# Kernel tuning notes

Hardware: AMD Instinct MI355X
Metric: run time of the kernel (lower is better)

Reference implementation:

```python
import jax, jax.numpy as jnp
import numpy as np

B, N, D_IN, D_OUT, H = 64, 512, 256, 256, 4
HD = D_OUT // H


def setup_inputs() -> dict:
    key = jax.random.key(0)
    ks = jax.random.split(key, 10)
    x = jax.random.normal(ks[0], (B, N, D_IN), dtype=jnp.float32)
    adj = jax.random.randint(ks[1], (N, N), 0, 2, dtype=jnp.int32)
    adj = adj.at[jnp.arange(N), jnp.arange(N)].set(1)  # self-loops: no empty rows
    s_in = 1.0 / np.sqrt(D_IN)
    s_out = 1.0 / np.sqrt(D_OUT)
    wq = jax.random.uniform(ks[2], (D_OUT, D_IN), jnp.float32, -s_in, s_in)
    bq = jax.random.uniform(ks[3], (D_OUT,), jnp.float32, -s_in, s_in)
    wk = jax.random.uniform(ks[4], (D_OUT, D_IN), jnp.float32, -s_in, s_in)
    bk = jax.random.uniform(ks[5], (D_OUT,), jnp.float32, -s_in, s_in)
    wv = jax.random.uniform(ks[6], (D_OUT, D_IN), jnp.float32, -s_in, s_in)
    bv = jax.random.uniform(ks[7], (D_OUT,), jnp.float32, -s_in, s_in)
    wo = jax.random.uniform(ks[8], (D_OUT, D_OUT), jnp.float32, -s_out, s_out)
    bo = jax.random.uniform(ks[9], (D_OUT,), jnp.float32, -s_out, s_out)
    return {"x": x, "adj": adj, "wq": wq, "bq": bq, "wk": wk, "bk": bk,
            "wv": wv, "bv": bv, "wo": wo, "bo": bo}


def reference(x, adj, wq, bq, wk, bk, wv, bv, wo, bo):
    b, n, _ = x.shape
    # [B,N,D_out] -> [B,H,N,HD]
    q = (x @ wq.T + bq).reshape(b, n, H, HD).transpose(0, 2, 1, 3)
    k = (x @ wk.T + bk).reshape(b, n, H, HD).transpose(0, 2, 1, 3)
    v = (x @ wv.T + bv).reshape(b, n, H, HD).transpose(0, 2, 1, 3)
    scores = jnp.einsum('bhnd,bhmd->bhnm', q, k) / jnp.sqrt(jnp.float32(HD))
    scores = jnp.where(adj[None, None] == 0, -jnp.inf, scores)
    attn = jnp.nan_to_num(jax.nn.softmax(scores, axis=-1), nan=0.0)
    out = jnp.einsum('bhnm,bhmd->bhnd', attn, v)
    out = out.transpose(0, 2, 1, 3).reshape(b, n, D_OUT)
    return out @ wo.T + bo
```

## Files before the change

kernel.cpp:

```cpp
#include <hip/hip_runtime.h>
#include <stdint.h>

typedef float f32x4 __attribute__((ext_vector_type(4)));
typedef short s16x8 __attribute__((ext_vector_type(8)));
typedef unsigned short u16x4 __attribute__((ext_vector_type(4)));

#define BB 64
#define NN 512
#define DIN 256
#define DOUT 256
#define HH 4
#define HD 64

__device__ __forceinline__ unsigned short f2b(float f) {
  union { float f; unsigned u; } v; v.f = f;
  unsigned r = v.u + 0x7fffu + ((v.u >> 16) & 1u);
  return (unsigned short)(r >> 16);
}
__device__ __forceinline__ void mfma16(f32x4& acc, s16x8 a, s16x8 b) {
  acc = __builtin_amdgcn_mfma_f32_16x16x32_bf16(a, b, acc, 0, 0, 0);
}
__device__ __forceinline__ unsigned cvtpk(float lo, float hi) {
  unsigned r;
  asm("v_cvt_pk_bf16_f32 %0, %1, %2" : "=v"(r) : "v"(lo), "v"(hi));
  return r;
}

__global__ void k_conv(const float* __restrict__ src, unsigned short* __restrict__ dst, int n4) {
  int i = blockIdx.x * blockDim.x + threadIdx.x;
  if (i >= n4) return;
  f32x4 v = ((const f32x4*)src)[i];
  u16x4 o;
  o[0] = f2b(v[0]); o[1] = f2b(v[1]); o[2] = f2b(v[2]); o[3] = f2b(v[3]);
  ((u16x4*)dst)[i] = o;
}

__global__ void k_adjbits(const int* __restrict__ adj, unsigned long long* __restrict__ ab) {
  int row = blockIdx.x;
  int w = threadIdx.x >> 6, lane = threadIdx.x & 63;
  int v = adj[row * NN + w * 64 + lane];
  unsigned long long m = __ballot(v != 0);
  if (lane == 0) ab[row * 8 + w] = m;
}

__global__ __launch_bounds__(256) void k_qkv(
    const unsigned short* __restrict__ xh,
    const unsigned short* __restrict__ wqh,
    const unsigned short* __restrict__ wkh,
    const unsigned short* __restrict__ wvh,
    const float* __restrict__ bq, const float* __restrict__ bk, const float* __restrict__ bv,
    unsigned short* __restrict__ Qb, unsigned short* __restrict__ Kb, unsigned short* __restrict__ Vtb)
{
  __shared__ __align__(16) unsigned char xs[32768];
  __shared__ __align__(16) unsigned char wsl[32768];
  int tid = threadIdx.x, wave = tid >> 6, lane = tid & 63;
  int lr = lane & 15, lk = lane >> 4;
  int t0 = blockIdx.x * 64;
  int by = blockIdx.y, seg = by >> 2, nb0 = (by & 3) * 64;
  const unsigned short* wh = seg == 0 ? wqh : (seg == 1 ? wkh : wvh);
  const float* bias = seg == 0 ? bq : (seg == 1 ? bk : bv);
  int h = by & 3;

  const unsigned short* xsrc = xh + (size_t)t0 * DIN;
  const unsigned short* wsrc = wh + (size_t)nb0 * DIN;
#pragma unroll
  for (int i = 0; i < 8; ++i) {
    int lin = i * 256 + tid;
    int r = lin >> 5, cc = lin & 31;
    int dst = r * 512 + ((cc ^ (r & 7)) << 4);
    *(s16x8*)(xs + dst)  = *(const s16x8*)(xsrc + lin * 8);
    *(s16x8*)(wsl + dst) = *(const s16x8*)(wsrc + lin * 8);
  }
  __syncthreads();

  f32x4 acc[4] = {};
  if (seg < 2) {
    int chrow = wave * 16 + lr;
#pragma unroll
    for (int k0 = 0; k0 < 8; ++k0) {
      int cg = k0 * 4 + lk;
      s16x8 a = *(const s16x8*)(wsl + chrow * 512 + ((cg ^ (chrow & 7)) << 4));
#pragma unroll
      for (int ct = 0; ct < 4; ++ct) {
        int tr = ct * 16 + lr;
        s16x8 b = *(const s16x8*)(xs + tr * 512 + ((cg ^ (tr & 7)) << 4));
        mfma16(acc[ct], a, b);
      }
    }
    unsigned short* dst = (seg == 0) ? Qb : Kb;
    f32x4 bv4 = *(const f32x4*)(bias + nb0 + wave * 16 + lk * 4);
#pragma unroll
    for (int ct = 0; ct < 4; ++ct) {
      int n_ = t0 + ct * 16 + lr;
      int b_ = n_ >> 9, nn = n_ & 511;
      u16x4 pk;
#pragma unroll
      for (int j = 0; j < 4; ++j) pk[j] = f2b(acc[ct][j] + bv4[j]);
      *(u16x4*)(dst + ((size_t)(b_ * HH + h) * NN + nn) * HD + wave * 16 + lk * 4) = pk;
    }
  } else {
    int tokrow = wave * 16 + lr;
#pragma unroll
    for (int k0 = 0; k0 < 8; ++k0) {
      int cg = k0 * 4 + lk;
      s16x8 a = *(const s16x8*)(xs + tokrow * 512 + ((cg ^ (tokrow & 7)) << 4));
#pragma unroll
      for (int nt = 0; nt < 4; ++nt) {
        int cr = nt * 16 + lr;
        s16x8 b = *(const s16x8*)(wsl + cr * 512 + ((cg ^ (cr & 7)) << 4));
        mfma16(acc[nt], a, b);
      }
    }
    int m0 = t0 + wave * 16 + lk * 4;
    int b_ = m0 >> 9, n0 = m0 & 511;
#pragma unroll
    for (int nt = 0; nt < 4; ++nt) {
      int hd = nt * 16 + lr;
      float bs = bias[nb0 + hd];
      u16x4 pk;
#pragma unroll
      for (int j = 0; j < 4; ++j) pk[j] = f2b(acc[nt][j] + bs);
      *(u16x4*)(Vtb + ((size_t)(b_ * HH + h) * HD + hd) * NN + n0) = pk;
    }
  }
}

__global__ __launch_bounds__(512, 2) void k_attn(
    const unsigned short* __restrict__ Qb, const unsigned short* __restrict__ Kb,
    const unsigned short* __restrict__ Vtb, const unsigned long long* __restrict__ ab,
    unsigned short* __restrict__ att)
{
  __shared__ __align__(16) unsigned char kl[2][8192];
  __shared__ __align__(16) unsigned char vtl[2][8192];
  __shared__ __align__(16) unsigned char plb[32768];

  int tid = threadIdx.x, wave = tid >> 6, lane = tid & 63;
  int lr = lane & 15, lk = lane >> 4;
  int bid = blockIdx.x;
  int g = bid >> 4, r = bid & 15;
  int bh = g * 8 + (r & 7);
  int qt = r >> 3;
  int h = bh & 3, b_ = bh >> 2;
  const unsigned short* Qp = Qb + (size_t)bh * NN * HD;
  const unsigned short* Kp = Kb + (size_t)bh * NN * HD;
  const unsigned short* Vp = Vtb + (size_t)bh * HD * NN;
  int q0 = qt * 256 + wave * 32;

  s16x8 qa[2][2];
#pragma unroll
  for (int s = 0; s < 2; ++s) {
    qa[s][0] = *(const s16x8*)(Qp + (q0 + s * 16 + lr) * HD + lk * 8);
    qa[s][1] = *(const s16x8*)(Qp + (q0 + s * 16 + lr) * HD + 32 + lk * 8);
  }

  f32x4 oacc[2][4] = {};
  float rs[2] = {0.f, 0.f};
  unsigned char* plw = plb + wave * 4096;
  int sw = (lr & 7) << 4;

  int srow = tid >> 3, scol = tid & 7;
  int sdst = srow * 128 + ((scol * 16) ^ ((srow & 7) << 4));
  const unsigned short* ksrc = Kp + srow * HD + scol * 8;
  const unsigned short* vsrc = Vp + srow * NN + scol * 8;

  *(s16x8*)(kl[0] + sdst)  = *(const s16x8*)ksrc;
  *(s16x8*)(vtl[0] + sdst) = *(const s16x8*)vsrc;
  __syncthreads();

#pragma unroll
  for (int kt = 0; kt < 8; ++kt) {
    unsigned char* klc = kl[kt & 1];
    unsigned char* vtc = vtl[kt & 1];
    unsigned long long abr[2];
#pragma unroll
    for (int s = 0; s < 2; ++s) abr[s] = ab[(size_t)(q0 + s * 16 + lr) * 8 + kt];

#pragma unroll
    for (int s = 0; s < 2; ++s) {
#pragma unroll
      for (int ks = 0; ks < 4; ++ks) {
        int key = ks * 16 + lr;
        s16x8 kb0 = *(const s16x8*)(klc + key * 128 + ((lk * 16) ^ ((key & 7) << 4)));
        s16x8 kb1 = *(const s16x8*)(klc + key * 128 + ((64 + lk * 16) ^ ((key & 7) << 4)));
        f32x4 sx = {};
        mfma16(sx, kb0, qa[s][0]);
        mfma16(sx, kb1, qa[s][1]);
        float p[4];
#pragma unroll
        for (int j = 0; j < 4; ++j)
          p[j] = ((abr[s] >> (ks * 16 + lk * 4 + j)) & 1ULL) ? __expf(sx[j] * 0.125f) : 0.0f;
        unsigned w0 = cvtpk(p[0], p[1]);
        unsigned w1 = cvtpk(p[2], p[3]);
        union { unsigned u; float f; } t0, t1, t2, t3;
        t0.u = w0 << 16; t1.u = w0 & 0xffff0000u;
        t2.u = w1 << 16; t3.u = w1 & 0xffff0000u;
        rs[s] += (t0.f + t1.f) + (t2.f + t3.f);
        uint2 pw; pw.x = w0; pw.y = w1;
        *(uint2*)(plw + s * 2048 + lr * 128 + ((ks * 32 + lk * 8) ^ sw)) = pw;
      }
    }

    s16x8 gk, gv;
    if (kt < 7) {
      gk = *(const s16x8*)(ksrc + (kt + 1) * 64 * HD);
      gv = *(const s16x8*)(vsrc + (kt + 1) * 64);
    }

#pragma unroll
    for (int s = 0; s < 2; ++s) {
      s16x8 pa0 = *(const s16x8*)(plw + s * 2048 + lr * 128 + ((lk * 16) ^ sw));
      s16x8 pa1 = *(const s16x8*)(plw + s * 2048 + lr * 128 + ((64 + lk * 16) ^ sw));
#pragma unroll
      for (int dt = 0; dt < 4; ++dt) {
        int d = dt * 16 + lr;
        s16x8 vb0 = *(const s16x8*)(vtc + d * 128 + ((lk * 16) ^ ((d & 7) << 4)));
        s16x8 vb1 = *(const s16x8*)(vtc + d * 128 + ((64 + lk * 16) ^ ((d & 7) << 4)));
        mfma16(oacc[s][dt], vb0, pa0);
        mfma16(oacc[s][dt], vb1, pa1);
      }
    }
    if (kt < 7) {
      *(s16x8*)(kl[(kt & 1) ^ 1] + sdst)  = gk;
      *(s16x8*)(vtl[(kt & 1) ^ 1] + sdst) = gv;
      __syncthreads();
    }
  }

#pragma unroll
  for (int s = 0; s < 2; ++s) {
    float v = rs[s];
    v += __shfl_xor(v, 16);
    v += __shfl_xor(v, 32);
    float rinv = 1.0f / v;
    int n_ = q0 + s * 16 + lr;
#pragma unroll
    for (int dt = 0; dt < 4; ++dt) {
      uint2 ow;
      ow.x = cvtpk(oacc[s][dt][0] * rinv, oacc[s][dt][1] * rinv);
      ow.y = cvtpk(oacc[s][dt][2] * rinv, oacc[s][dt][3] * rinv);
      *(uint2*)(att + ((size_t)(b_ * NN + n_) * DOUT) + h * HD + dt * 16 + lk * 4) = ow;
    }
  }
}

__global__ __launch_bounds__(256) void k_out(
    const unsigned short* __restrict__ att, const unsigned short* __restrict__ woh,
    const float* __restrict__ bo, float* __restrict__ out)
{
  __shared__ __align__(16) unsigned char as_[32768];
  __shared__ __align__(16) unsigned char wsl[32768];
  int tid = threadIdx.x, wave = tid >> 6, lane = tid & 63;
  int lr = lane & 15, lk = lane >> 4;
  int t0 = blockIdx.x * 64;
  int nb0 = blockIdx.y * 64;

  const unsigned short* asrc = att + (size_t)t0 * DOUT;
  const unsigned short* wsrc = woh + (size_t)nb0 * DOUT;
#pragma unroll
  for (int i = 0; i < 8; ++i) {
    int lin = i * 256 + tid;
    int r = lin >> 5, cc = lin & 31;
    int dst = r * 512 + ((cc ^ (r & 7)) << 4);
    *(s16x8*)(as_ + dst) = *(const s16x8*)(asrc + lin * 8);
    *(s16x8*)(wsl + dst) = *(const s16x8*)(wsrc + lin * 8);
  }
  __syncthreads();

  f32x4 acc[4] = {};
  int chrow = wave * 16 + lr;
#pragma unroll
  for (int k0 = 0; k0 < 8; ++k0) {
    int cg = k0 * 4 + lk;
    s16x8 a = *(const s16x8*)(wsl + chrow * 512 + ((cg ^ (chrow & 7)) << 4));
#pragma unroll
    for (int ct = 0; ct < 4; ++ct) {
      int tr = ct * 16 + lr;
      s16x8 b = *(const s16x8*)(as_ + tr * 512 + ((cg ^ (tr & 7)) << 4));
      mfma16(acc[ct], a, b);
    }
  }
  f32x4 bv4 = *(const f32x4*)(bo + nb0 + wave * 16 + lk * 4);
#pragma unroll
  for (int ct = 0; ct < 4; ++ct) {
    int m = t0 + ct * 16 + lr;
    f32x4 o = acc[ct] + bv4;
    *(f32x4*)(out + (size_t)m * DOUT + nb0 + wave * 16 + lk * 4) = o;
  }
}

extern "C" void kernel_launch(void* const* d_in, const int* in_sizes, int n_in,
                              void* d_out, int out_size, void* d_ws, size_t ws_size,
                              hipStream_t stream) {
  const float* x  = (const float*)d_in[0];
  const int*   adj = (const int*)d_in[1];
  const float* wq = (const float*)d_in[2];
  const float* bq = (const float*)d_in[3];
  const float* wk = (const float*)d_in[4];
  const float* bk = (const float*)d_in[5];
  const float* wv = (const float*)d_in[6];
  const float* bv = (const float*)d_in[7];
  const float* wo = (const float*)d_in[8];
  const float* bo = (const float*)d_in[9];
  float* out = (float*)d_out;

  char* ws = (char*)d_ws;
  size_t off = 0;
  auto carve = [&](size_t bytes) -> char* {
    off = (off + 255) & ~(size_t)255;
    char* p = ws + off;
    off += bytes;
    return p;
  };
  unsigned short* xh   = (unsigned short*)carve((size_t)BB * NN * DIN * 2);
  unsigned short* wqh  = (unsigned short*)carve((size_t)DOUT * DIN * 2);
  unsigned short* wkh  = (unsigned short*)carve((size_t)DOUT * DIN * 2);
  unsigned short* wvh  = (unsigned short*)carve((size_t)DOUT * DIN * 2);
  unsigned short* woh  = (unsigned short*)carve((size_t)DOUT * DOUT * 2);
  unsigned long long* abits = (unsigned long long*)carve((size_t)NN * 8 * 8);
  unsigned short* Qb   = (unsigned short*)carve((size_t)BB * HH * NN * HD * 2);
  unsigned short* Kb   = (unsigned short*)carve((size_t)BB * HH * NN * HD * 2);
  unsigned short* Vtb  = (unsigned short*)carve((size_t)BB * HH * HD * NN * 2);
  unsigned short* attb = (unsigned short*)carve((size_t)BB * NN * DOUT * 2);

  k_conv<<<dim3(8192), 256, 0, stream>>>(x, xh, (BB * NN * DIN) / 4);
  k_conv<<<dim3(64), 256, 0, stream>>>(wq, wqh, (DOUT * DIN) / 4);
  k_conv<<<dim3(64), 256, 0, stream>>>(wk, wkh, (DOUT * DIN) / 4);
  k_conv<<<dim3(64), 256, 0, stream>>>(wv, wvh, (DOUT * DIN) / 4);
  k_conv<<<dim3(64), 256, 0, stream>>>(wo, woh, (DOUT * DOUT) / 4);
  k_adjbits<<<dim3(512), 512, 0, stream>>>(adj, abits);
  k_qkv<<<dim3(512, 12), 256, 0, stream>>>(xh, wqh, wkh, wvh, bq, bk, bv, Qb, Kb, Vtb);
  k_attn<<<dim3(512), 512, 0, stream>>>(Qb, Kb, Vtb, abits, attb);
  k_out<<<dim3(512, 4), 256, 0, stream>>>(attb, woh, bo, out);
}
```

Measured before the change: 201.1 us.

## Fuse x bf16 conversion into QKV GEMM and loop weight chunks per block

Removes the separate fp32-to-bf16 pass over x by converting inside k_qkv's LDS staging. Each QKV block now keeps its x tile resident and loops over all 12 weight chunks, prefetching the next chunk into registers while computing. The four weight conversion launches are merged into one, and k_out likewise loops over its 4 weight chunks per block. This cuts global traffic for x and removes launches, but leaves only 512 blocks per GEMM kernel and adds serial per-block work and extra barriers.

```diff
diff --git a/kernel.cpp b/kernel.cpp
--- a/kernel.cpp
+++ b/kernel.cpp
@@ -4,6 +4,7 @@
 typedef float f32x4 __attribute__((ext_vector_type(4)));
 typedef short s16x8 __attribute__((ext_vector_type(8)));
 typedef unsigned short u16x4 __attribute__((ext_vector_type(4)));
+typedef unsigned int u32x4 __attribute__((ext_vector_type(4)));
 
 #define BB 64
 #define NN 512
@@ -26,13 +27,19 @@
   return r;
 }
 
-__global__ void k_conv(const float* __restrict__ src, unsigned short* __restrict__ dst, int n4) {
-  int i = blockIdx.x * blockDim.x + threadIdx.x;
-  if (i >= n4) return;
-  f32x4 v = ((const f32x4*)src)[i];
+__global__ void k_wconv(const float* __restrict__ s0, const float* __restrict__ s1,
+                        const float* __restrict__ s2, const float* __restrict__ s3,
+                        unsigned short* __restrict__ d0, unsigned short* __restrict__ d1,
+                        unsigned short* __restrict__ d2, unsigned short* __restrict__ d3) {
+  int b = blockIdx.x;
+  int mat = b >> 6;
+  int i = (b & 63) * 256 + threadIdx.x;
+  const float* s = mat == 0 ? s0 : mat == 1 ? s1 : mat == 2 ? s2 : s3;
+  unsigned short* d = mat == 0 ? d0 : mat == 1 ? d1 : mat == 2 ? d2 : d3;
+  f32x4 v = ((const f32x4*)s)[i];
   u16x4 o;
   o[0] = f2b(v[0]); o[1] = f2b(v[1]); o[2] = f2b(v[2]); o[3] = f2b(v[3]);
-  ((u16x4*)dst)[i] = o;
+  ((u16x4*)d)[i] = o;
 }
 
 __global__ void k_adjbits(const int* __restrict__ adj, unsigned long long* __restrict__ ab) {
@@ -43,8 +50,8 @@
   if (lane == 0) ab[row * 8 + w] = m;
 }
 
-__global__ __launch_bounds__(256) void k_qkv(
-    const unsigned short* __restrict__ xh,
+__global__ __launch_bounds__(256, 2) void k_qkv(
+    const float* __restrict__ x,
     const unsigned short* __restrict__ wqh,
     const unsigned short* __restrict__ wkh,
     const unsigned short* __restrict__ wvh,
@@ -56,72 +63,95 @@
   int tid = threadIdx.x, wave = tid >> 6, lane = tid & 63;
   int lr = lane & 15, lk = lane >> 4;
   int t0 = blockIdx.x * 64;
-  int by = blockIdx.y, seg = by >> 2, nb0 = (by & 3) * 64;
-  const unsigned short* wh = seg == 0 ? wqh : (seg == 1 ? wkh : wvh);
-  const float* bias = seg == 0 ? bq : (seg == 1 ? bk : bv);
-  int h = by & 3;
-
-  const unsigned short* xsrc = xh + (size_t)t0 * DIN;
-  const unsigned short* wsrc = wh + (size_t)nb0 * DIN;
+
+  const float* xsrc = x + (size_t)t0 * DIN;
 #pragma unroll
   for (int i = 0; i < 8; ++i) {
     int lin = i * 256 + tid;
     int r = lin >> 5, cc = lin & 31;
     int dst = r * 512 + ((cc ^ (r & 7)) << 4);
-    *(s16x8*)(xs + dst)  = *(const s16x8*)(xsrc + lin * 8);
-    *(s16x8*)(wsl + dst) = *(const s16x8*)(wsrc + lin * 8);
+    f32x4 a = *(const f32x4*)(xsrc + lin * 8);
+    f32x4 b = *(const f32x4*)(xsrc + lin * 8 + 4);
+    u32x4 pk;
+    pk[0] = cvtpk(a[0], a[1]); pk[1] = cvtpk(a[2], a[3]);
+    pk[2] = cvtpk(b[0], b[1]); pk[3] = cvtpk(b[2], b[3]);
+    *(u32x4*)(xs + dst) = pk;
+    *(s16x8*)(wsl + dst) = *(const s16x8*)(wqh + lin * 8);
   }
   __syncthreads();
 
-  f32x4 acc[4] = {};
-  if (seg < 2) {
-    int chrow = wave * 16 + lr;
-#pragma unroll
-    for (int k0 = 0; k0 < 8; ++k0) {
-      int cg = k0 * 4 + lk;
-      s16x8 a = *(const s16x8*)(wsl + chrow * 512 + ((cg ^ (chrow & 7)) << 4));
+  for (int c = 0; c < 12; ++c) {
+    int seg = c >> 2, h = c & 3, nb0 = h * 64;
+    const float* bias = seg == 0 ? bq : (seg == 1 ? bk : bv);
+
+    s16x8 gw[8];
+    if (c < 11) {
+      int cn = c + 1, segn = cn >> 2;
+      const unsigned short* wn = (segn == 0 ? wqh : segn == 1 ? wkh : wvh) + (size_t)(cn & 3) * 64 * DIN;
+#pragma unroll
+      for (int i = 0; i < 8; ++i) gw[i] = *(const s16x8*)(wn + (i * 256 + tid) * 8);
+    }
+
+    f32x4 acc[4] = {};
+    if (seg < 2) {
+      int chrow = wave * 16 + lr;
+#pragma unroll
+      for (int k0 = 0; k0 < 8; ++k0) {
+        int cg = k0 * 4 + lk;
+        s16x8 a = *(const s16x8*)(wsl + chrow * 512 + ((cg ^ (chrow & 7)) << 4));
+#pragma unroll
+        for (int ct = 0; ct < 4; ++ct) {
+          int tr = ct * 16 + lr;
+          s16x8 b = *(const s16x8*)(xs + tr * 512 + ((cg ^ (tr & 7)) << 4));
+          mfma16(acc[ct], a, b);
+        }
+      }
+      unsigned short* dst = (seg == 0) ? Qb : Kb;
+      f32x4 bv4 = *(const f32x4*)(bias + nb0 + wave * 16 + lk * 4);
 #pragma unroll
       for (int ct = 0; ct < 4; ++ct) {
-        int tr = ct * 16 + lr;
-        s16x8 b = *(const s16x8*)(xs + tr * 512 + ((cg ^ (tr & 7)) << 4));
-        mfma16(acc[ct], a, b);
-      }
-    }
-    unsigned short* dst = (seg == 0) ? Qb : Kb;
-    f32x4 bv4 = *(const f32x4*)(bias + nb0 + wave * 16 + lk * 4);
-#pragma unroll
-    for (int ct = 0; ct < 4; ++ct) {
-      int n_ = t0 + ct * 16 + lr;
-      int b_ = n_ >> 9, nn = n_ & 511;
-      u16x4 pk;
-#pragma unroll
-      for (int j = 0; j < 4; ++j) pk[j] = f2b(acc[ct][j] + bv4[j]);
-      *(u16x4*)(dst + ((size_t)(b_ * HH + h) * NN + nn) * HD + wave * 16 + lk * 4) = pk;
-    }
-  } else {
-    int tokrow = wave * 16 + lr;
-#pragma unroll
-    for (int k0 = 0; k0 < 8; ++k0) {
-      int cg = k0 * 4 + lk;
-      s16x8 a = *(const s16x8*)(xs + tokrow * 512 + ((cg ^ (tokrow & 7)) << 4));
+        int n_ = t0 + ct * 16 + lr;
+        int b_ = n_ >> 9, nn = n_ & 511;
+        u16x4 pk;
+#pragma unroll
+        for (int j = 0; j < 4; ++j) pk[j] = f2b(acc[ct][j] + bv4[j]);
+        *(u16x4*)(dst + ((size_t)(b_ * HH + h) * NN + nn) * HD + wave * 16 + lk * 4) = pk;
+      }
+    } else {
+      int tokrow = wave * 16 + lr;
+#pragma unroll
+      for (int k0 = 0; k0 < 8; ++k0) {
+        int cg = k0 * 4 + lk;
+        s16x8 a = *(const s16x8*)(xs + tokrow * 512 + ((cg ^ (tokrow & 7)) << 4));
+#pragma unroll
+        for (int nt = 0; nt < 4; ++nt) {
+          int cr = nt * 16 + lr;
+          s16x8 b = *(const s16x8*)(wsl + cr * 512 + ((cg ^ (cr & 7)) << 4));
+          mfma16(acc[nt], a, b);
+        }
+      }
+      int m0 = t0 + wave * 16 + lk * 4;
+      int b_ = m0 >> 9, n0 = m0 & 511;
 #pragma unroll
       for (int nt = 0; nt < 4; ++nt) {
-        int cr = nt * 16 + lr;
-        s16x8 b = *(const s16x8*)(wsl + cr * 512 + ((cg ^ (cr & 7)) << 4));
-        mfma16(acc[nt], a, b);
-      }
-    }
-    int m0 = t0 + wave * 16 + lk * 4;
-    int b_ = m0 >> 9, n0 = m0 & 511;
-#pragma unroll
-    for (int nt = 0; nt < 4; ++nt) {
-      int hd = nt * 16 + lr;
-      float bs = bias[nb0 + hd];
-      u16x4 pk;
-#pragma unroll
-      for (int j = 0; j < 4; ++j) pk[j] = f2b(acc[nt][j] + bs);
-      *(u16x4*)(Vtb + ((size_t)(b_ * HH + h) * HD + hd) * NN + n0) = pk;
-    }
+        int hd = nt * 16 + lr;
+        float bs = bias[nb0 + hd];
+        u16x4 pk;
+#pragma unroll
+        for (int j = 0; j < 4; ++j) pk[j] = f2b(acc[nt][j] + bs);
+        *(u16x4*)(Vtb + ((size_t)(b_ * HH + h) * HD + hd) * NN + n0) = pk;
+      }
+    }
+    __syncthreads();
+    if (c < 11) {
+#pragma unroll
+      for (int i = 0; i < 8; ++i) {
+        int lin = i * 256 + tid;
+        int r = lin >> 5, cc = lin & 31;
+        *(s16x8*)(wsl + r * 512 + ((cc ^ (r & 7)) << 4)) = gw[i];
+      }
+    }
+    __syncthreads();
   }
 }
 
@@ -243,7 +273,7 @@
   }
 }
 
-__global__ __launch_bounds__(256) void k_out(
+__global__ __launch_bounds__(256, 2) void k_out(
     const unsigned short* __restrict__ att, const unsigned short* __restrict__ woh,
     const float* __restrict__ bo, float* __restrict__ out)
 {
@@ -252,39 +282,57 @@
   int tid = threadIdx.x, wave = tid >> 6, lane = tid & 63;
   int lr = lane & 15, lk = lane >> 4;
   int t0 = blockIdx.x * 64;
-  int nb0 = blockIdx.y * 64;
 
   const unsigned short* asrc = att + (size_t)t0 * DOUT;
-  const unsigned short* wsrc = woh + (size_t)nb0 * DOUT;
 #pragma unroll
   for (int i = 0; i < 8; ++i) {
     int lin = i * 256 + tid;
     int r = lin >> 5, cc = lin & 31;
     int dst = r * 512 + ((cc ^ (r & 7)) << 4);
     *(s16x8*)(as_ + dst) = *(const s16x8*)(asrc + lin * 8);
-    *(s16x8*)(wsl + dst) = *(const s16x8*)(wsrc + lin * 8);
+    *(s16x8*)(wsl + dst) = *(const s16x8*)(woh + lin * 8);
   }
   __syncthreads();
 
-  f32x4 acc[4] = {};
-  int chrow = wave * 16 + lr;
-#pragma unroll
-  for (int k0 = 0; k0 < 8; ++k0) {
-    int cg = k0 * 4 + lk;
-    s16x8 a = *(const s16x8*)(wsl + chrow * 512 + ((cg ^ (chrow & 7)) << 4));
+  for (int c = 0; c < 4; ++c) {
+    int nb0 = c * 64;
+    s16x8 gw[8];
+    if (c < 3) {
+      const unsigned short* wn = woh + (size_t)(c + 1) * 64 * DOUT;
+#pragma unroll
+      for (int i = 0; i < 8; ++i) gw[i] = *(const s16x8*)(wn + (i * 256 + tid) * 8);
+    }
+
+    f32x4 acc[4] = {};
+    int chrow = wave * 16 + lr;
+#pragma unroll
+    for (int k0 = 0; k0 < 8; ++k0) {
+      int cg = k0 * 4 + lk;
+      s16x8 a = *(const s16x8*)(wsl + chrow * 512 + ((cg ^ (chrow & 7)) << 4));
+#pragma unroll
+      for (int ct = 0; ct < 4; ++ct) {
+        int tr = ct * 16 + lr;
+        s16x8 b = *(const s16x8*)(as_ + tr * 512 + ((cg ^ (tr & 7)) << 4));
+        mfma16(acc[ct], a, b);
+      }
+    }
+    f32x4 bv4 = *(const f32x4*)(bo + nb0 + wave * 16 + lk * 4);
 #pragma unroll
     for (int ct = 0; ct < 4; ++ct) {
-      int tr = ct * 16 + lr;
-      s16x8 b = *(const s16x8*)(as_ + tr * 512 + ((cg ^ (tr & 7)) << 4));
-      mfma16(acc[ct], a, b);
-    }
-  }
-  f32x4 bv4 = *(const f32x4*)(bo + nb0 + wave * 16 + lk * 4);
-#pragma unroll
-  for (int ct = 0; ct < 4; ++ct) {
-    int m = t0 + ct * 16 + lr;
-    f32x4 o = acc[ct] + bv4;
-    *(f32x4*)(out + (size_t)m * DOUT + nb0 + wave * 16 + lk * 4) = o;
+      int m = t0 + ct * 16 + lr;
+      f32x4 o = acc[ct] + bv4;
+      *(f32x4*)(out + (size_t)m * DOUT + nb0 + wave * 16 + lk * 4) = o;
+    }
+    __syncthreads();
+    if (c < 3) {
+#pragma unroll
+      for (int i = 0; i < 8; ++i) {
+        int lin = i * 256 + tid;
+        int r = lin >> 5, cc = lin & 31;
+        *(s16x8*)(wsl + r * 512 + ((cc ^ (r & 7)) << 4)) = gw[i];
+      }
+    }
+    __syncthreads();
   }
 }
 
@@ -311,7 +359,6 @@
     off += bytes;
     return p;
   };
-  unsigned short* xh   = (unsigned short*)carve((size_t)BB * NN * DIN * 2);
   unsigned short* wqh  = (unsigned short*)carve((size_t)DOUT * DIN * 2);
   unsigned short* wkh  = (unsigned short*)carve((size_t)DOUT * DIN * 2);
   unsigned short* wvh  = (unsigned short*)carve((size_t)DOUT * DIN * 2);
@@ -322,13 +369,9 @@
   unsigned short* Vtb  = (unsigned short*)carve((size_t)BB * HH * HD * NN * 2);
   unsigned short* attb = (unsigned short*)carve((size_t)BB * NN * DOUT * 2);
 
-  k_conv<<<dim3(8192), 256, 0, stream>>>(x, xh, (BB * NN * DIN) / 4);
-  k_conv<<<dim3(64), 256, 0, stream>>>(wq, wqh, (DOUT * DIN) / 4);
-  k_conv<<<dim3(64), 256, 0, stream>>>(wk, wkh, (DOUT * DIN) / 4);
-  k_conv<<<dim3(64), 256, 0, stream>>>(wv, wvh, (DOUT * DIN) / 4);
-  k_conv<<<dim3(64), 256, 0, stream>>>(wo, woh, (DOUT * DOUT) / 4);
+  k_wconv<<<dim3(256), 256, 0, stream>>>(wq, wk, wv, wo, wqh, wkh, wvh, woh);
   k_adjbits<<<dim3(512), 512, 0, stream>>>(adj, abits);
-  k_qkv<<<dim3(512, 12), 256, 0, stream>>>(xh, wqh, wkh, wvh, bq, bk, bv, Qb, Kb, Vtb);
+  k_qkv<<<dim3(512), 256, 0, stream>>>(x, wqh, wkh, wvh, bq, bk, bv, Qb, Kb, Vtb);
   k_attn<<<dim3(512), 512, 0, stream>>>(Qb, Kb, Vtb, abits, attb);
-  k_out<<<dim3(512, 4), 256, 0, stream>>>(attb, woh, bo, out);
-}
+  k_out<<<dim3(512), 256, 0, stream>>>(attb, woh, bo, out);
+}
```

New measurement: 181.5 us. 9.7% less time.
